# Optimization experiments

Hardware: AMD Instinct MI355X
Metric: run time of the kernel (lower is better)

Reference implementation:

```python
import jax, jax.numpy as jnp
import numpy as np

DELTA_A, DELTA_R = 0.1, 1.0
ALPHA, BETA, GAMMA = 1.0, 1.0, 0.001


def setup_inputs() -> dict:
    key = jax.random.key(0)
    B, D, H, W, K = 4, 32, 512, 512, 16
    out = jax.random.normal(key, (B, D, H, W), dtype=jnp.float32)
    # 4x4 block partition -> K=16 instance labels, one center per block
    gh, gw = 4, 4
    bh, bw = H // gh, W // gw
    rows = np.arange(H) // bh  # [H]
    cols = np.arange(W) // bw  # [W]
    labels = (rows[:, None] * gw + cols[None, :]).astype(np.int32)  # [H,W]
    target = jnp.asarray(np.broadcast_to(labels, (B, H, W)).copy())
    ctr = np.array([[r * bh + bh // 2, c * bw + bw // 2]
                    for r in range(gh) for c in range(gw)], dtype=np.int32)  # [K,2]
    centers = jnp.asarray(np.broadcast_to(ctr, (B, K, 2)).copy())
    return {"out": out, "target": target, "centers": centers, "batch_size": B}


def _safe_sqrt(x):
    # matches torch.linalg.norm subgradient 0 at 0 (avoids NaN grads)
    pos = x > 0
    return jnp.where(pos, jnp.sqrt(jnp.where(pos, x, 1.0)), 0.0)


def _pairwise_norm(a, b):
    # a [M,D], b [N,D] -> [M,N] euclidean distances via gram trick
    d2 = (jnp.sum(a * a, 1)[:, None] + jnp.sum(b * b, 1)[None, :]
          - 2.0 * a @ b.T)
    return _safe_sqrt(jax.nn.relu(d2))


def _per_image(o, t, c):
    # o [D,H,W], t [H,W] int, c [K,2] int
    D = o.shape[0]
    K = c.shape[0]
    x = o.reshape(D, -1).T                      # [HW, D]
    E = o[:, c[:, 0], c[:, 1]].T                # [K, D] center embeddings
    lab_c = t[c[:, 0], c[:, 1]]                 # [K]
    mask = (t.reshape(-1)[None, :] == lab_c[:, None])  # [K, HW]
    # attraction: hinged distance of every cluster pixel to its center
    norms = _pairwise_norm(E, x)                # [K, HW]
    hinged = jax.nn.relu(norms - DELTA_A) * mask
    cnt = jnp.sum(mask, axis=1)
    denom = jnp.maximum(cnt - 1, 1).astype(o.dtype)
    s_att = jnp.sum(jnp.sum(hinged, axis=1) / denom)
    # repelling: pairwise center distances; diagonal contributes relu(delta_r)
    # per row and the original subtracts delta_r per center -> excluded
    nE = _pairwise_norm(E, E)                   # [K, K]
    s_rep = jnp.sum(jax.nn.relu(DELTA_R - nE)) - K * DELTA_R
    # regularization: norm of each center embedding
    s_reg = jnp.sum(_safe_sqrt(jnp.sum(E * E, axis=1)))
    return s_att, s_rep, s_reg


def reference(out, target, centers, batch_size):
    K = centers.shape[1]
    s_att, s_rep, s_reg = jax.vmap(_per_image)(out, target, centers)  # [B] each
    div_att = jnp.float32(K)
    div_rep = jnp.float32(K * (K - 1))
    div_reg = jnp.float32(K)

    def step(carry, s):
        a, r, g = carry
        sa, sr, sg = s
        return ((a + sa) / div_att, (r + sr) / div_rep, (g + sg) / div_reg), None

    zero = jnp.float32(0.0)
    (att, rep, reg), _ = jax.lax.scan(step, (zero, zero, zero),
                                      (s_att, s_rep, s_reg))
    loss = ALPHA * att + BETA * rep + GAMMA * reg
    return loss, att, rep
```

## Files before the change

### kernel.cpp

```cpp
#include <hip/hip_runtime.h>
#include <hip/hip_bf16.h>

#define B_ 4
#define D_ 32
#define H_ 512
#define W_ 512
#define K_ 16
#define N_ (H_ * W_)
#define NQ_ (N_ / 4)
#define NBLK_ 256
#define EPAD 33

#define WS_SUM  0
#define WS_CNT  64
#define WS_E2   128
#define WS_LAB  192
#define WS_E    264
#define WS_PART 4096

typedef float vfloat4 __attribute__((ext_vector_type(4)));
typedef int vint4 __attribute__((ext_vector_type(4)));

__device__ inline vfloat4 nt_load_f4(const float* p) {
  return __builtin_nontemporal_load((const vfloat4*)p);
}
__device__ inline vint4 nt_load_i4(const int* p) {
  return __builtin_nontemporal_load((const vint4*)p);
}

__global__ __launch_bounds__(64) void setup_kernel(
    const float* __restrict__ outp, const int* __restrict__ target,
    const int* __restrict__ centers, float* __restrict__ ws) {
  const int b = blockIdx.x, k = blockIdx.y;
  const int lane = threadIdx.x;
  const int cy = centers[(b * K_ + k) * 2 + 0];
  const int cx = centers[(b * K_ + k) * 2 + 1];
  float v = 0.0f;
  if (lane < D_) {
    v = outp[(((size_t)b * D_ + lane) * H_ + cy) * W_ + cx];
    ws[WS_E + (b * K_ + k) * D_ + lane] = v;
  }
  float s = v * v;
  for (int off = 32; off > 0; off >>= 1) s += __shfl_xor(s, off, 64);
  if (lane == 0) {
    ws[WS_E2 + b * K_ + k] = s;
    ((int*)ws)[WS_LAB + b * K_ + k] = target[(size_t)b * N_ + cy * W_ + cx];
  }
}

__global__ __launch_bounds__(256, 4) void attract_kernel(
    const float* __restrict__ outp, const int* __restrict__ target,
    float* __restrict__ ws) {
  const int b = blockIdx.y;
  const int tid = threadIdx.x;
  __shared__ float sE[K_ * EPAD];
  __shared__ float se2[K_];
  __shared__ int slab[K_];
  __shared__ float bs[K_];
  __shared__ float bc[K_];

  if (tid < 128) {
    const vfloat4 v = *(const vfloat4*)(ws + WS_E + b * (K_ * D_) + tid * 4);
    const int k = tid >> 3, d = (tid & 7) * 4;
    sE[k * EPAD + d + 0] = v.x;
    sE[k * EPAD + d + 1] = v.y;
    sE[k * EPAD + d + 2] = v.z;
    sE[k * EPAD + d + 3] = v.w;
  }
  if (tid < K_) {
    se2[tid] = ws[WS_E2 + b * K_ + tid];
    slab[tid] = ((const int*)ws)[WS_LAB + b * K_ + tid];
    bs[tid] = 0.0f;
    bc[tid] = 0.0f;
  }
  __syncthreads();

  const int q = blockIdx.x * 256 + tid;
  const float* xb = outp + (size_t)b * D_ * N_;
  const vint4 lab4 = nt_load_i4(target + (size_t)b * N_ + 4 * q);
  const int labv[4] = {lab4.x, lab4.y, lab4.z, lab4.w};

  int kf[4], nm[4];
#pragma unroll
  for (int j = 0; j < 4; ++j) { kf[j] = 0; nm[j] = 0; }
#pragma unroll
  for (int k = 0; k < K_; ++k) {
    const int lk = slab[k];
#pragma unroll
    for (int j = 0; j < 4; ++j) {
      if (labv[j] == lk) { if (nm[j] == 0) kf[j] = k; nm[j]++; }
    }
  }

  const int lane = tid & 63;
  const bool thread_ok =
      (nm[0] == 1) & (nm[1] == 1) & (nm[2] == 1) & (nm[3] == 1) &
      (kf[1] == kf[0]) & (kf[2] == kf[0]) & (kf[3] == kf[0]);
  const int kA = __builtin_amdgcn_readfirstlane(kf[0]);
  const int kB = __shfl(kf[0], 32, 64);
  const bool low = lane < 32;
  const bool half_ok = kf[0] == (low ? kA : kB);
  const bool fast = __all(thread_ok & half_ok);

  if (fast) {
    const float* __restrict__ eA = ws + WS_E + (b * K_ + kA) * D_;
    const float* __restrict__ eB = ws + WS_E + (b * K_ + __builtin_amdgcn_readfirstlane(kB)) * D_;
    float dot[4] = {0.f, 0.f, 0.f, 0.f};
    float x2[4] = {0.f, 0.f, 0.f, 0.f};
#pragma unroll 8
    for (int d = 0; d < D_; ++d) {
      const vfloat4 x = nt_load_f4(xb + (size_t)d * N_ + 4 * q);
      const float e = low ? eA[d] : eB[d];
      dot[0] = fmaf(x.x, e, dot[0]);
      x2[0] = fmaf(x.x, x.x, x2[0]);
      dot[1] = fmaf(x.y, e, dot[1]);
      x2[1] = fmaf(x.y, x.y, x2[1]);
      dot[2] = fmaf(x.z, e, dot[2]);
      x2[2] = fmaf(x.z, x.z, x2[2]);
      dot[3] = fmaf(x.w, e, dot[3]);
      x2[3] = fmaf(x.w, x.w, x2[3]);
    }
    const float e2k = se2[kf[0]];
    float hq = 0.0f;
#pragma unroll
    for (int j = 0; j < 4; ++j) {
      const float d2 = x2[j] + e2k - 2.0f * dot[j];
      hq += fmaxf(sqrtf(fmaxf(d2, 0.0f)) - 0.1f, 0.0f);
    }
    for (int off = 16; off > 0; off >>= 1) hq += __shfl_xor(hq, off, 64);
    if ((lane & 31) == 0) {
      atomicAdd(&bs[kf[0]], hq);
      atomicAdd(&bc[kf[0]], 128.0f);
    }
  } else {
    float dot[4] = {0.f, 0.f, 0.f, 0.f};
    float x2[4] = {0.f, 0.f, 0.f, 0.f};
#pragma unroll 8
    for (int d = 0; d < D_; ++d) {
      const vfloat4 x = nt_load_f4(xb + (size_t)d * N_ + 4 * q);
      const float xs[4] = {x.x, x.y, x.z, x.w};
#pragma unroll
      for (int j = 0; j < 4; ++j) {
        const float e = sE[kf[j] * EPAD + d];
        dot[j] = fmaf(xs[j], e, dot[j]);
        x2[j] = fmaf(xs[j], xs[j], x2[j]);
      }
    }
#pragma unroll
    for (int j = 0; j < 4; ++j) {
      if (nm[j] > 0) {
        const float d2 = x2[j] + se2[kf[j]] - 2.0f * dot[j];
        atomicAdd(&bs[kf[j]], fmaxf(sqrtf(fmaxf(d2, 0.0f)) - 0.1f, 0.0f));
        atomicAdd(&bc[kf[j]], 1.0f);
      }
    }
    const bool extra = (nm[0] > 1) | (nm[1] > 1) | (nm[2] > 1) | (nm[3] > 1);
    if (__any(extra)) {
      for (int k = 0; k < K_; ++k) {
        bool need[4]; bool anyn = false;
#pragma unroll
        for (int j = 0; j < 4; ++j) {
          need[j] = (nm[j] > 1) && (labv[j] == slab[k]) && (k != kf[j]);
          anyn |= need[j];
        }
        if (__any(anyn)) {
          float dt[4] = {0.f, 0.f, 0.f, 0.f};
          for (int d = 0; d < D_; ++d) {
            const vfloat4 x = nt_load_f4(xb + (size_t)d * N_ + 4 * q);
            const float e = sE[k * EPAD + d];
            dt[0] = fmaf(x.x, e, dt[0]);
            dt[1] = fmaf(x.y, e, dt[1]);
            dt[2] = fmaf(x.z, e, dt[2]);
            dt[3] = fmaf(x.w, e, dt[3]);
          }
#pragma unroll
          for (int j = 0; j < 4; ++j) {
            if (need[j]) {
              const float d2 = x2[j] + se2[k] - 2.0f * dt[j];
              atomicAdd(&bs[k], fmaxf(sqrtf(fmaxf(d2, 0.0f)) - 0.1f, 0.0f));
              atomicAdd(&bc[k], 1.0f);
            }
          }
        }
      }
    }
  }
  __syncthreads();

  if (tid < 2 * K_) {
    float* p = ws + WS_PART + ((size_t)b * NBLK_ + blockIdx.x) * (2 * K_);
    p[tid] = (tid < K_) ? bs[tid] : bc[tid - K_];
  }
}

__global__ __launch_bounds__(256) void final_kernel(const float* __restrict__ ws,
                                                    float* __restrict__ out) {
  __shared__ float sE[B_ * K_ * D_];
  __shared__ float sred[256];
  __shared__ float scred[256];
  __shared__ float ssum[B_ * K_];
  __shared__ float scnt[B_ * K_];
  __shared__ float srep[B_];
  __shared__ float sreg[B_];
  __shared__ float ssa[B_];
  const int tid = threadIdx.x;

  {
    const int p = tid >> 2, sub = tid & 3;
    const int bb = p >> 4, kk = p & 15;
    const float* base = ws + WS_PART + (size_t)bb * NBLK_ * (2 * K_);
    float s = 0.0f, c = 0.0f;
    for (int i = sub; i < NBLK_; i += 4) {
      s += base[i * (2 * K_) + kk];
      c += base[i * (2 * K_) + K_ + kk];
    }
    sred[tid] = s;
    scred[tid] = c;
  }
  for (int i = tid; i < B_ * K_ * D_; i += 256) sE[i] = ws[WS_E + i];
  __syncthreads();
  if (tid < B_ * K_) {
    ssum[tid] = sred[tid * 4] + sred[tid * 4 + 1] + sred[tid * 4 + 2] + sred[tid * 4 + 3];
    scnt[tid] = scred[tid * 4] + scred[tid * 4 + 1] + scred[tid * 4 + 2] + scred[tid * 4 + 3];
  }
  __syncthreads();

  const int i = tid >> 4, j = tid & 15;
  for (int b = 0; b < B_; ++b) {
    float dotv = 0.0f;
#pragma unroll 8
    for (int d = 0; d < D_; ++d)
      dotv = fmaf(sE[(b * K_ + i) * D_ + d], sE[(b * K_ + j) * D_ + d], dotv);
    const float d2 = ws[WS_E2 + b * K_ + i] + ws[WS_E2 + b * K_ + j] - 2.0f * dotv;
    sred[tid] = fmaxf(1.0f - sqrtf(fmaxf(d2, 0.0f)), 0.0f);
    __syncthreads();
    for (int s = 128; s > 0; s >>= 1) {
      if (tid < s) sred[tid] += sred[tid + s];
      __syncthreads();
    }
    if (tid == 0) srep[b] = sred[0] - (float)K_;
    __syncthreads();
  }

  sred[tid] = (tid < B_ * K_) ? sqrtf(fmaxf(ws[WS_E2 + tid], 0.0f)) : 0.0f;
  __syncthreads();
  if (tid < B_) {
    float s = 0.0f;
    for (int k = 0; k < K_; ++k) s += sred[tid * K_ + k];
    sreg[tid] = s;
  }

  if (tid < B_ * K_) {
    float v = ssum[tid] / fmaxf(scnt[tid] - 1.0f, 1.0f);
    for (int off = 1; off < K_; off <<= 1) v += __shfl_xor(v, off, 64);
    if ((tid & 15) == 0) ssa[tid >> 4] = v;
  }
  __syncthreads();

  if (tid == 0) {
    float att = 0.0f, rep = 0.0f, reg = 0.0f;
    for (int b = 0; b < B_; ++b) {
      att = (att + ssa[b]) / (float)K_;
      rep = (rep + srep[b]) / (float)(K_ * (K_ - 1));
      reg = (reg + sreg[b]) / (float)K_;
    }
    out[0] = att + rep + 0.001f * reg;
    out[1] = att;
    out[2] = rep;
  }
}

extern "C" void kernel_launch(void* const* d_in, const int* in_sizes, int n_in,
                              void* d_out, int out_size, void* d_ws, size_t ws_size,
                              hipStream_t stream) {
  const float* outp = (const float*)d_in[0];
  const int* target = (const int*)d_in[1];
  const int* centers = (const int*)d_in[2];
  float* ws = (float*)d_ws;
  float* out = (float*)d_out;

  setup_kernel<<<dim3(B_, K_), 64, 0, stream>>>(outp, target, centers, ws);
  attract_kernel<<<dim3(NBLK_, B_), 256, 0, stream>>>(outp, target, ws);
  final_kernel<<<1, 256, 0, stream>>>(ws, out);
}
```

Measured before the change: 220.2 us.

## Process eight pixels per thread with direct squared-difference distance in fast path

Each thread now handles 8 consecutive pixels with two float4 loads per channel, halving the grid to 128 blocks per image. The fast path computes the distance directly as a sum of squared differences from the center, instead of using the gram expansion, and reads center values from shared memory. It also checks label uniformity first, so the full label-matching loop only runs in the slow path. Fewer blocks and more registers per thread trade occupancy for more memory-level parallelism per thread, and the launch bound's occupancy hint is dropped.

```diff
diff --git a/kernel.cpp b/kernel.cpp
--- a/kernel.cpp
+++ b/kernel.cpp
@@ -7,8 +7,8 @@
 #define W_ 512
 #define K_ 16
 #define N_ (H_ * W_)
-#define NQ_ (N_ / 4)
-#define NBLK_ 256
+#define NO8_ (N_ / 8)
+#define NB2_ 128
 #define EPAD 33
 
 #define WS_SUM  0
@@ -48,7 +48,7 @@
   }
 }
 
-__global__ __launch_bounds__(256, 4) void attract_kernel(
+__global__ __launch_bounds__(256) void attract_kernel(
     const float* __restrict__ outp, const int* __restrict__ target,
     float* __restrict__ ws) {
   const int b = blockIdx.y;
@@ -75,106 +75,118 @@
   }
   __syncthreads();
 
-  const int q = blockIdx.x * 256 + tid;
+  const int g = blockIdx.x * 256 + tid;
   const float* xb = outp + (size_t)b * D_ * N_;
-  const vint4 lab4 = nt_load_i4(target + (size_t)b * N_ + 4 * q);
-  const int labv[4] = {lab4.x, lab4.y, lab4.z, lab4.w};
-
-  int kf[4], nm[4];
-#pragma unroll
-  for (int j = 0; j < 4; ++j) { kf[j] = 0; nm[j] = 0; }
-#pragma unroll
-  for (int k = 0; k < K_; ++k) {
-    const int lk = slab[k];
-#pragma unroll
-    for (int j = 0; j < 4; ++j) {
-      if (labv[j] == lk) { if (nm[j] == 0) kf[j] = k; nm[j]++; }
-    }
-  }
-
+  const int* tb = target + (size_t)b * N_;
+  const vint4 la = nt_load_i4(tb + 8 * g);
+  const vint4 lb = nt_load_i4(tb + 8 * g + 4);
+  const int lab[8] = {la.x, la.y, la.z, la.w, lb.x, lb.y, lb.z, lb.w};
+
+  bool alleq = true;
+#pragma unroll
+  for (int j = 1; j < 8; ++j) alleq &= (lab[j] == lab[0]);
+
+  int kf0 = 0, nm0 = 0;
+  if (alleq) {
+#pragma unroll
+    for (int k = 0; k < K_; ++k) {
+      if (lab[0] == slab[k]) { if (nm0 == 0) kf0 = k; nm0++; }
+    }
+  }
   const int lane = tid & 63;
-  const bool thread_ok =
-      (nm[0] == 1) & (nm[1] == 1) & (nm[2] == 1) & (nm[3] == 1) &
-      (kf[1] == kf[0]) & (kf[2] == kf[0]) & (kf[3] == kf[0]);
-  const int kA = __builtin_amdgcn_readfirstlane(kf[0]);
-  const int kB = __shfl(kf[0], 32, 64);
-  const bool low = lane < 32;
-  const bool half_ok = kf[0] == (low ? kA : kB);
-  const bool fast = __all(thread_ok & half_ok);
-
-  if (fast) {
-    const float* __restrict__ eA = ws + WS_E + (b * K_ + kA) * D_;
-    const float* __restrict__ eB = ws + WS_E + (b * K_ + __builtin_amdgcn_readfirstlane(kB)) * D_;
-    float dot[4] = {0.f, 0.f, 0.f, 0.f};
-    float x2[4] = {0.f, 0.f, 0.f, 0.f};
+  const int kg = __shfl(kf0, lane & ~15, 64);
+  const bool ok = alleq && (nm0 == 1) && (kf0 == kg);
+
+  if (__all(ok)) {
+    float acc[8] = {0.f, 0.f, 0.f, 0.f, 0.f, 0.f, 0.f, 0.f};
 #pragma unroll 8
     for (int d = 0; d < D_; ++d) {
-      const vfloat4 x = nt_load_f4(xb + (size_t)d * N_ + 4 * q);
-      const float e = low ? eA[d] : eB[d];
-      dot[0] = fmaf(x.x, e, dot[0]);
-      x2[0] = fmaf(x.x, x.x, x2[0]);
-      dot[1] = fmaf(x.y, e, dot[1]);
-      x2[1] = fmaf(x.y, x.y, x2[1]);
-      dot[2] = fmaf(x.z, e, dot[2]);
-      x2[2] = fmaf(x.z, x.z, x2[2]);
-      dot[3] = fmaf(x.w, e, dot[3]);
-      x2[3] = fmaf(x.w, x.w, x2[3]);
-    }
-    const float e2k = se2[kf[0]];
+      const vfloat4 xa = nt_load_f4(xb + (size_t)d * N_ + 8 * g);
+      const vfloat4 xc = nt_load_f4(xb + (size_t)d * N_ + 8 * g + 4);
+      const float e = sE[kf0 * EPAD + d];
+      const float v0 = xa.x - e, v1 = xa.y - e, v2 = xa.z - e, v3 = xa.w - e;
+      const float v4 = xc.x - e, v5 = xc.y - e, v6 = xc.z - e, v7 = xc.w - e;
+      acc[0] = fmaf(v0, v0, acc[0]);
+      acc[1] = fmaf(v1, v1, acc[1]);
+      acc[2] = fmaf(v2, v2, acc[2]);
+      acc[3] = fmaf(v3, v3, acc[3]);
+      acc[4] = fmaf(v4, v4, acc[4]);
+      acc[5] = fmaf(v5, v5, acc[5]);
+      acc[6] = fmaf(v6, v6, acc[6]);
+      acc[7] = fmaf(v7, v7, acc[7]);
+    }
     float hq = 0.0f;
 #pragma unroll
-    for (int j = 0; j < 4; ++j) {
-      const float d2 = x2[j] + e2k - 2.0f * dot[j];
-      hq += fmaxf(sqrtf(fmaxf(d2, 0.0f)) - 0.1f, 0.0f);
-    }
-    for (int off = 16; off > 0; off >>= 1) hq += __shfl_xor(hq, off, 64);
-    if ((lane & 31) == 0) {
-      atomicAdd(&bs[kf[0]], hq);
-      atomicAdd(&bc[kf[0]], 128.0f);
+    for (int j = 0; j < 8; ++j)
+      hq += fmaxf(sqrtf(acc[j]) - 0.1f, 0.0f);
+    hq += __shfl_xor(hq, 1, 64);
+    hq += __shfl_xor(hq, 2, 64);
+    hq += __shfl_xor(hq, 4, 64);
+    hq += __shfl_xor(hq, 8, 64);
+    if ((lane & 15) == 0) {
+      atomicAdd(&bs[kf0], hq);
+      atomicAdd(&bc[kf0], 128.0f);
     }
   } else {
-    float dot[4] = {0.f, 0.f, 0.f, 0.f};
-    float x2[4] = {0.f, 0.f, 0.f, 0.f};
-#pragma unroll 8
+    int kf[8], nm[8];
+#pragma unroll
+    for (int j = 0; j < 8; ++j) { kf[j] = 0; nm[j] = 0; }
+#pragma unroll
+    for (int k = 0; k < K_; ++k) {
+      const int lk = slab[k];
+#pragma unroll
+      for (int j = 0; j < 8; ++j) {
+        if (lab[j] == lk) { if (nm[j] == 0) kf[j] = k; nm[j]++; }
+      }
+    }
+    float dot[8], x2[8];
+#pragma unroll
+    for (int j = 0; j < 8; ++j) { dot[j] = 0.f; x2[j] = 0.f; }
+#pragma unroll 4
     for (int d = 0; d < D_; ++d) {
-      const vfloat4 x = nt_load_f4(xb + (size_t)d * N_ + 4 * q);
-      const float xs[4] = {x.x, x.y, x.z, x.w};
-#pragma unroll
-      for (int j = 0; j < 4; ++j) {
+      const vfloat4 xa = nt_load_f4(xb + (size_t)d * N_ + 8 * g);
+      const vfloat4 xc = nt_load_f4(xb + (size_t)d * N_ + 8 * g + 4);
+      const float xs[8] = {xa.x, xa.y, xa.z, xa.w, xc.x, xc.y, xc.z, xc.w};
+#pragma unroll
+      for (int j = 0; j < 8; ++j) {
         const float e = sE[kf[j] * EPAD + d];
         dot[j] = fmaf(xs[j], e, dot[j]);
         x2[j] = fmaf(xs[j], xs[j], x2[j]);
       }
     }
 #pragma unroll
-    for (int j = 0; j < 4; ++j) {
+    for (int j = 0; j < 8; ++j) {
       if (nm[j] > 0) {
         const float d2 = x2[j] + se2[kf[j]] - 2.0f * dot[j];
         atomicAdd(&bs[kf[j]], fmaxf(sqrtf(fmaxf(d2, 0.0f)) - 0.1f, 0.0f));
         atomicAdd(&bc[kf[j]], 1.0f);
       }
     }
-    const bool extra = (nm[0] > 1) | (nm[1] > 1) | (nm[2] > 1) | (nm[3] > 1);
-    if (__any(extra)) {
+    bool anyextra = false;
+#pragma unroll
+    for (int j = 0; j < 8; ++j) anyextra |= (nm[j] > 1);
+    if (__any(anyextra)) {
       for (int k = 0; k < K_; ++k) {
-        bool need[4]; bool anyn = false;
-#pragma unroll
-        for (int j = 0; j < 4; ++j) {
-          need[j] = (nm[j] > 1) && (labv[j] == slab[k]) && (k != kf[j]);
+        bool need[8]; bool anyn = false;
+#pragma unroll
+        for (int j = 0; j < 8; ++j) {
+          need[j] = (nm[j] > 1) && (lab[j] == slab[k]) && (k != kf[j]);
           anyn |= need[j];
         }
         if (__any(anyn)) {
-          float dt[4] = {0.f, 0.f, 0.f, 0.f};
+          float dt[8];
+#pragma unroll
+          for (int j = 0; j < 8; ++j) dt[j] = 0.f;
           for (int d = 0; d < D_; ++d) {
-            const vfloat4 x = nt_load_f4(xb + (size_t)d * N_ + 4 * q);
+            const vfloat4 xa = nt_load_f4(xb + (size_t)d * N_ + 8 * g);
+            const vfloat4 xc = nt_load_f4(xb + (size_t)d * N_ + 8 * g + 4);
+            const float xs[8] = {xa.x, xa.y, xa.z, xa.w, xc.x, xc.y, xc.z, xc.w};
             const float e = sE[k * EPAD + d];
-            dt[0] = fmaf(x.x, e, dt[0]);
-            dt[1] = fmaf(x.y, e, dt[1]);
-            dt[2] = fmaf(x.z, e, dt[2]);
-            dt[3] = fmaf(x.w, e, dt[3]);
+#pragma unroll
+            for (int j = 0; j < 8; ++j) dt[j] = fmaf(xs[j], e, dt[j]);
           }
 #pragma unroll
-          for (int j = 0; j < 4; ++j) {
+          for (int j = 0; j < 8; ++j) {
             if (need[j]) {
               const float d2 = x2[j] + se2[k] - 2.0f * dt[j];
               atomicAdd(&bs[k], fmaxf(sqrtf(fmaxf(d2, 0.0f)) - 0.1f, 0.0f));
@@ -188,7 +200,7 @@
   __syncthreads();
 
   if (tid < 2 * K_) {
-    float* p = ws + WS_PART + ((size_t)b * NBLK_ + blockIdx.x) * (2 * K_);
+    float* p = ws + WS_PART + ((size_t)b * NB2_ + blockIdx.x) * (2 * K_);
     p[tid] = (tid < K_) ? bs[tid] : bc[tid - K_];
   }
 }
@@ -208,9 +220,9 @@
   {
     const int p = tid >> 2, sub = tid & 3;
     const int bb = p >> 4, kk = p & 15;
-    const float* base = ws + WS_PART + (size_t)bb * NBLK_ * (2 * K_);
+    const float* base = ws + WS_PART + (size_t)bb * NB2_ * (2 * K_);
     float s = 0.0f, c = 0.0f;
-    for (int i = sub; i < NBLK_; i += 4) {
+    for (int i = sub; i < NB2_; i += 4) {
       s += base[i * (2 * K_) + kk];
       c += base[i * (2 * K_) + K_ + kk];
     }
@@ -280,6 +292,6 @@
   float* out = (float*)d_out;
 
   setup_kernel<<<dim3(B_, K_), 64, 0, stream>>>(outp, target, centers, ws);
-  attract_kernel<<<dim3(NBLK_, B_), 256, 0, stream>>>(outp, target, ws);
+  attract_kernel<<<dim3(NB2_, B_), 256, 0, stream>>>(outp, target, ws);
   final_kernel<<<1, 256, 0, stream>>>(ws, out);
 }
```

After: 206.6 us. 6.2% less time.
